# Optimization experiments

Hardware: AMD Instinct MI355X
Metric: run time of the kernel (lower is better)

The kernel has to match this reference:

```python
import jax, jax.numpy as jnp
import numpy as np

N_NODES = 50000
N_EDGES = 400000
IN_CH = 7
EMBED = 128
EDGE_DIM = 6


def setup_inputs() -> dict:
    key = jax.random.key(0)
    ks = jax.random.split(key, 10)
    x = jax.random.normal(ks[0], (N_NODES, IN_CH), dtype=jnp.float32)
    edge_index = jax.random.randint(ks[1], (2, N_EDGES), 0, N_NODES, dtype=jnp.int64)
    edge_attr = jax.random.normal(ks[2], (N_EDGES, EDGE_DIM), dtype=jnp.float32)
    # edge MLP params: Linear(6,128) -> GELU -> Linear(128, 7*128)
    s1 = 1.0 / np.sqrt(EDGE_DIM)
    s2 = 1.0 / np.sqrt(EMBED)
    W1 = jax.random.uniform(ks[3], (EDGE_DIM, EMBED), jnp.float32, -s1, s1)
    b1 = jax.random.uniform(ks[4], (EMBED,), jnp.float32, -s1, s1)
    W2 = jax.random.uniform(ks[5], (EMBED, IN_CH * EMBED), jnp.float32, -s2, s2)
    b2 = jax.random.uniform(ks[6], (IN_CH * EMBED,), jnp.float32, -s2, s2)
    # NNConv root weight and bias
    s3 = 1.0 / np.sqrt(IN_CH)
    root = jax.random.uniform(ks[7], (IN_CH, EMBED), jnp.float32, -s3, s3)
    bias = jnp.zeros((EMBED,), dtype=jnp.float32)
    return {"x": x, "edge_index": edge_index, "edge_attr": edge_attr,
            "W1": W1, "b1": b1, "W2": W2, "b2": b2, "root": root, "bias": bias}


def reference(x, edge_index, edge_attr, W1, b1, W2, b2, root, bias):
    N = x.shape[0]
    src, dst = edge_index[0], edge_index[1]
    # edge MLP -> per-edge weight matrix [E, in_ch, embed]
    h = jax.nn.gelu(edge_attr @ W1 + b1, approximate=False)
    w = (h @ W2 + b2).reshape(-1, IN_CH, EMBED)
    # gather source node features, per-edge small matmul
    msg = jnp.einsum('ei,eio->eo', x[src], w)  # [E, embed]
    # mean aggregation at target nodes
    summed = jax.ops.segment_sum(msg, dst, num_segments=N)
    cnt = jax.ops.segment_sum(jnp.ones((msg.shape[0],), msg.dtype), dst, num_segments=N)
    aggr = summed / jnp.clip(cnt, 1.0)[:, None]
    return aggr + x @ root + bias
```

## Files before the change

kernel.cpp:

```cpp
#include <hip/hip_runtime.h>
#include <stdint.h>

#define NNODES 50000
#define NEDGES 400000
#define INCH 7
#define EMB 128
#define EDIM 6
#define KD 896
#define BM 128
#define NSTEPS 28

typedef __attribute__((ext_vector_type(8))) short bf16x8;
typedef __attribute__((ext_vector_type(4))) float f32x4;

__device__ __forceinline__ short f2bf(float f) {
  union { float f; uint32_t u; } v; v.f = f;
  uint32_t r = v.u + 0x7FFFu + ((v.u >> 16) & 1u);
  return (short)(r >> 16);
}

__global__ void prep_B(const float* __restrict__ W2, short* __restrict__ Bg) {
  int idx = blockIdx.x * 256 + threadIdx.x;
  int o = idx / KD;
  int c = idx - o * KD;
  int i = c >> 7, k = c & 127;
  Bg[idx] = f2bf(W2[k * KD + (i << 7) + o]);
}

__device__ __forceinline__ void stageB(short* dstB, const short* __restrict__ Bg,
                                       int step, int w, int lane) {
#pragma unroll
  for (int j = 0; j < 2; ++j) {
    const int row = w * 32 + j * 16 + (lane >> 2);
    const char* g = (const char*)Bg + (size_t)row * (KD * 2) + step * 64 + (lane & 3) * 16;
    char* l = (char*)dstB + (w * 32 + j * 16) * 64;
    __builtin_amdgcn_global_load_lds((const __attribute__((address_space(1))) void*)g,
                                     (__attribute__((address_space(3))) void*)l,
                                     16, 0, 0);
  }
}

__global__ __launch_bounds__(256, 2)
void nnconv_main(const float* __restrict__ x,
                 const int* __restrict__ ei,
                 const float* __restrict__ ea,
                 const float* __restrict__ W1,
                 const float* __restrict__ b1,
                 const float* __restrict__ b2,
                 const short* __restrict__ Bg,
                 float* __restrict__ cnt,
                 float* __restrict__ out) {
  __shared__ __align__(16) short h_s[BM * EMB];
  __shared__ __align__(16) short B_s[2][EMB * 32];
  __shared__ __align__(16) float x_s[BM][8];
  __shared__ __align__(16) float ea_s[BM * EDIM];
  __shared__ __align__(16) float w1_s[EDIM * EMB];
  __shared__ __align__(16) float b1_s[EMB];
  __shared__ __align__(16) float b2_s[KD];
  __shared__ int dst_s[BM];

  const int t = threadIdx.x;
  const int lane = t & 63;
  const int w = t >> 6;
  const int eb = blockIdx.x * BM;

  if (t < 192) {
    *(float4*)&ea_s[t * 4] = *(const float4*)&ea[(size_t)eb * EDIM + t * 4];
    *(float4*)&w1_s[t * 4] = *(const float4*)&W1[t * 4];
  }
  if (t >= 192 && t < 224) { int q = t - 192; *(float4*)&b1_s[q * 4] = *(const float4*)&b1[q * 4]; }
  if (t < 224) *(float4*)&b2_s[t * 4] = *(const float4*)&b2[t * 4];
  if (t < BM) {
    int s = ei[eb + t];
    int d = ei[NEDGES + eb + t];
    dst_s[t] = d;
#pragma unroll
    for (int i = 0; i < 7; ++i) x_s[t][i] = x[s * 7 + i];
    atomicAdd(&cnt[d], 1.0f);
  }
  stageB(&B_s[0][0], Bg, 0, w, lane);
  __syncthreads();

  {
    const int e = t >> 1, half = t & 1;
    float a[6];
#pragma unroll
    for (int q = 0; q < 6; ++q) a[q] = ea_s[e * 6 + q];
    const int swz = (e & 7) << 4;
#pragma unroll
    for (int j = 0; j < 8; ++j) {
      bf16x8 hv;
#pragma unroll
      for (int m = 0; m < 8; ++m) {
        int c = half * 64 + j * 8 + m;
        float pre = b1_s[c];
#pragma unroll
        for (int q = 0; q < 6; ++q) pre += a[q] * w1_s[q * EMB + c];
        float g = 0.5f * pre * (1.0f + erff(pre * 0.70710678118f));
        hv[m] = f2bf(g);
      }
      int addr = e * 256 + ((half * 128 + j * 16) ^ swz);
      *(bf16x8*)((char*)h_s + addr) = hv;
    }
  }
  asm volatile("s_waitcnt vmcnt(0)" ::: "memory");
  __syncthreads();

  const int wm = w >> 1, wn = w & 1;
  const int rowA = lane & 15;
  const int kseg = lane >> 4;

  f32x4 acc[4][4];
#pragma unroll
  for (int fm = 0; fm < 4; ++fm)
#pragma unroll
    for (int fn = 0; fn < 4; ++fn) acc[fm][fn] = f32x4{0.f, 0.f, 0.f, 0.f};

  int cur = 0;
#pragma unroll 1
  for (int i = 0; i < 7; ++i) {
    f32x4 tmp[4][4];
#pragma unroll
    for (int fm = 0; fm < 4; ++fm)
#pragma unroll
      for (int fn = 0; fn < 4; ++fn) tmp[fm][fn] = f32x4{0.f, 0.f, 0.f, 0.f};

#pragma unroll
    for (int kk = 0; kk < 4; ++kk) {
      const int step = i * 4 + kk;
      if (step < NSTEPS - 1) stageB(&B_s[cur ^ 1][0], Bg, step + 1, w, lane);

      bf16x8 af[4], bfr[4];
#pragma unroll
      for (int fm = 0; fm < 4; ++fm) {
        int row = wm * 64 + fm * 16 + rowA;
        int col = (kk * 64 + kseg * 16) ^ ((row & 7) << 4);
        af[fm] = *(const bf16x8*)((const char*)h_s + row * 256 + col);
      }
#pragma unroll
      for (int fn = 0; fn < 4; ++fn) {
        int n = wn * 64 + fn * 16 + rowA;
        bfr[fn] = *(const bf16x8*)((const char*)&B_s[cur][0] + n * 64 + kseg * 16);
      }
#pragma unroll
      for (int fm = 0; fm < 4; ++fm)
#pragma unroll
        for (int fn = 0; fn < 4; ++fn)
          tmp[fm][fn] = __builtin_amdgcn_mfma_f32_16x16x32_bf16(af[fm], bfr[fn], tmp[fm][fn], 0, 0, 0);

      asm volatile("s_waitcnt vmcnt(0)" ::: "memory");
      __syncthreads();
      cur ^= 1;
    }
#pragma unroll
    for (int fm = 0; fm < 4; ++fm) {
#pragma unroll
      for (int r = 0; r < 4; ++r) {
        float xv = x_s[wm * 64 + fm * 16 + kseg * 4 + r][i];
#pragma unroll
        for (int fn = 0; fn < 4; ++fn) acc[fm][fn][r] += xv * tmp[fm][fn][r];
      }
    }
  }

  const int colA = rowA;
  float bb[4][7];
#pragma unroll
  for (int fn = 0; fn < 4; ++fn)
#pragma unroll
    for (int i = 0; i < 7; ++i) bb[fn][i] = b2_s[i * EMB + wn * 64 + fn * 16 + colA];

#pragma unroll
  for (int fm = 0; fm < 4; ++fm) {
#pragma unroll
    for (int r = 0; r < 4; ++r) {
      const int row = wm * 64 + fm * 16 + kseg * 4 + r;
      float xr[7];
#pragma unroll
      for (int i = 0; i < 7; ++i) xr[i] = x_s[row][i];
      const int d = dst_s[row];
      float* op = out + (size_t)d * EMB + wn * 64 + colA;
#pragma unroll
      for (int fn = 0; fn < 4; ++fn) {
        float v = acc[fm][fn][r];
#pragma unroll
        for (int i = 0; i < 7; ++i) v += xr[i] * bb[fn][i];
        atomicAdd(op + fn * 16, v);
      }
    }
  }
}

__global__ void finalize(const float* __restrict__ x, const float* __restrict__ root,
                         const float* __restrict__ bias, const float* __restrict__ cnt,
                         float* __restrict__ out) {
  int idx = blockIdx.x * 256 + threadIdx.x;
  int n = idx >> 7, o = idx & 127;
  float c = fmaxf(cnt[n], 1.0f);
  float v = out[idx] / c + bias[o];
#pragma unroll
  for (int i = 0; i < 7; ++i) v += x[n * 7 + i] * root[i * EMB + o];
  out[idx] = v;
}

extern "C" void kernel_launch(void* const* d_in, const int* in_sizes, int n_in,
                              void* d_out, int out_size, void* d_ws, size_t ws_size,
                              hipStream_t stream) {
  const float* x    = (const float*)d_in[0];
  const int*   ei   = (const int*)d_in[1];
  const float* ea   = (const float*)d_in[2];
  const float* W1   = (const float*)d_in[3];
  const float* b1   = (const float*)d_in[4];
  const float* W2   = (const float*)d_in[5];
  const float* b2   = (const float*)d_in[6];
  const float* root = (const float*)d_in[7];
  const float* bias = (const float*)d_in[8];
  float* out = (float*)d_out;

  short* Bg  = (short*)d_ws;
  float* cnt = (float*)((char*)d_ws + 128 * KD * 2);

  hipMemsetAsync(out, 0, (size_t)NNODES * EMB * sizeof(float), stream);
  hipMemsetAsync(cnt, 0, (size_t)NNODES * sizeof(float), stream);
  prep_B<<<448, 256, 0, stream>>>(W2, Bg);
  nnconv_main<<<NEDGES / BM, 256, 0, stream>>>(x, ei, ea, W1, b1, b2, Bg, cnt, out);
  finalize<<<NNODES * EMB / 256, 256, 0, stream>>>(x, root, bias, cnt, out);
}
```

Measured before the change: 363.3 us.

## Load pre-swizzled B fragments directly to registers and use tanh GELU

The prep kernel now writes W2 in MFMA fragment order, so each lane can load its B operand straight from global/L2 into registers with double-buffered prefetch. This removes the LDS staging of B and the per-k-step barriers. GELU switches from erf to a tanh approximation built on __expf, which cuts transcendental cost but changes numerics slightly. The h_s swizzle is widened to 16 rows and x_s is padded to reduce LDS bank conflicts.

```diff
diff --git a/kernel.cpp b/kernel.cpp
--- a/kernel.cpp
+++ b/kernel.cpp
@@ -19,25 +19,25 @@
   return (short)(r >> 16);
 }
 
-__global__ void prep_B(const float* __restrict__ W2, short* __restrict__ Bg) {
+__device__ __forceinline__ float fast_gelu(float x) {
+  float x2 = x * x;
+  float y = x * (0.7978845608f + 0.03567740814f * x2);
+  float e = __expf(2.0f * y);
+  float t = 1.0f - 2.0f / (1.0f + e);
+  return 0.5f * x * (1.0f + t);
+}
+
+__global__ void prep_B(const float* __restrict__ W2, short* __restrict__ Bp) {
   int idx = blockIdx.x * 256 + threadIdx.x;
-  int o = idx / KD;
-  int c = idx - o * KD;
-  int i = c >> 7, k = c & 127;
-  Bg[idx] = f2bf(W2[k * KD + (i << 7) + o]);
-}
-
-__device__ __forceinline__ void stageB(short* dstB, const short* __restrict__ Bg,
-                                       int step, int w, int lane) {
-#pragma unroll
-  for (int j = 0; j < 2; ++j) {
-    const int row = w * 32 + j * 16 + (lane >> 2);
-    const char* g = (const char*)Bg + (size_t)row * (KD * 2) + step * 64 + (lane & 3) * 16;
-    char* l = (char*)dstB + (w * 32 + j * 16) * 64;
-    __builtin_amdgcn_global_load_lds((const __attribute__((address_space(1))) void*)g,
-                                     (__attribute__((address_space(3))) void*)l,
-                                     16, 0, 0);
-  }
+  int m    = idx & 7;
+  int r    = (idx >> 3) & 15;
+  int kseg = (idx >> 7) & 3;
+  int nh   = (idx >> 9) & 7;
+  int step = idx >> 12;
+  int i = step >> 2, kk = step & 3;
+  int k = kk * 32 + kseg * 8 + m;
+  int o = nh * 16 + r;
+  Bp[idx] = f2bf(W2[k * KD + i * EMB + o]);
 }
 
 __global__ __launch_bounds__(256, 2)
@@ -47,12 +47,11 @@
                  const float* __restrict__ W1,
                  const float* __restrict__ b1,
                  const float* __restrict__ b2,
-                 const short* __restrict__ Bg,
+                 const short* __restrict__ Bp,
                  float* __restrict__ cnt,
                  float* __restrict__ out) {
   __shared__ __align__(16) short h_s[BM * EMB];
-  __shared__ __align__(16) short B_s[2][EMB * 32];
-  __shared__ __align__(16) float x_s[BM][8];
+  __shared__ __align__(16) float x_s[BM][9];
   __shared__ __align__(16) float ea_s[BM * EDIM];
   __shared__ __align__(16) float w1_s[EDIM * EMB];
   __shared__ __align__(16) float b1_s[EMB];
@@ -78,7 +77,6 @@
     for (int i = 0; i < 7; ++i) x_s[t][i] = x[s * 7 + i];
     atomicAdd(&cnt[d], 1.0f);
   }
-  stageB(&B_s[0][0], Bg, 0, w, lane);
   __syncthreads();
 
   {
@@ -86,7 +84,7 @@
     float a[6];
 #pragma unroll
     for (int q = 0; q < 6; ++q) a[q] = ea_s[e * 6 + q];
-    const int swz = (e & 7) << 4;
+    const int swz = (e & 15) << 4;
 #pragma unroll
     for (int j = 0; j < 8; ++j) {
       bf16x8 hv;
@@ -96,19 +94,18 @@
         float pre = b1_s[c];
 #pragma unroll
         for (int q = 0; q < 6; ++q) pre += a[q] * w1_s[q * EMB + c];
-        float g = 0.5f * pre * (1.0f + erff(pre * 0.70710678118f));
-        hv[m] = f2bf(g);
+        hv[m] = f2bf(fast_gelu(pre));
       }
       int addr = e * 256 + ((half * 128 + j * 16) ^ swz);
       *(bf16x8*)((char*)h_s + addr) = hv;
     }
   }
-  asm volatile("s_waitcnt vmcnt(0)" ::: "memory");
   __syncthreads();
 
   const int wm = w >> 1, wn = w & 1;
   const int rowA = lane & 15;
   const int kseg = lane >> 4;
+  const char* BpByte = (const char*)Bp + (size_t)lane * 16;
 
   f32x4 acc[4][4];
 #pragma unroll
@@ -116,7 +113,11 @@
 #pragma unroll
     for (int fn = 0; fn < 4; ++fn) acc[fm][fn] = f32x4{0.f, 0.f, 0.f, 0.f};
 
-  int cur = 0;
+  bf16x8 bcur[4], bnxt[4];
+#pragma unroll
+  for (int fn = 0; fn < 4; ++fn)
+    bcur[fn] = *(const bf16x8*)(BpByte + ((0 * 8 + wn * 4 + fn) << 10));
+
 #pragma unroll 1
   for (int i = 0; i < 7; ++i) {
     f32x4 tmp[4][4];
@@ -128,29 +129,25 @@
 #pragma unroll
     for (int kk = 0; kk < 4; ++kk) {
       const int step = i * 4 + kk;
-      if (step < NSTEPS - 1) stageB(&B_s[cur ^ 1][0], Bg, step + 1, w, lane);
-
-      bf16x8 af[4], bfr[4];
+      if (step < NSTEPS - 1) {
+#pragma unroll
+        for (int fn = 0; fn < 4; ++fn)
+          bnxt[fn] = *(const bf16x8*)(BpByte + (((step + 1) * 8 + wn * 4 + fn) << 10));
+      }
+      bf16x8 af[4];
 #pragma unroll
       for (int fm = 0; fm < 4; ++fm) {
         int row = wm * 64 + fm * 16 + rowA;
-        int col = (kk * 64 + kseg * 16) ^ ((row & 7) << 4);
+        int col = (kk * 64 + kseg * 16) ^ ((row & 15) << 4);
         af[fm] = *(const bf16x8*)((const char*)h_s + row * 256 + col);
       }
 #pragma unroll
-      for (int fn = 0; fn < 4; ++fn) {
-        int n = wn * 64 + fn * 16 + rowA;
-        bfr[fn] = *(const bf16x8*)((const char*)&B_s[cur][0] + n * 64 + kseg * 16);
-      }
-#pragma unroll
       for (int fm = 0; fm < 4; ++fm)
 #pragma unroll
         for (int fn = 0; fn < 4; ++fn)
-          tmp[fm][fn] = __builtin_amdgcn_mfma_f32_16x16x32_bf16(af[fm], bfr[fn], tmp[fm][fn], 0, 0, 0);
-
-      asm volatile("s_waitcnt vmcnt(0)" ::: "memory");
-      __syncthreads();
-      cur ^= 1;
+          tmp[fm][fn] = __builtin_amdgcn_mfma_f32_16x16x32_bf16(af[fm], bcur[fn], tmp[fm][fn], 0, 0, 0);
+#pragma unroll
+      for (int fn = 0; fn < 4; ++fn) bcur[fn] = bnxt[fn];
     }
 #pragma unroll
     for (int fm = 0; fm < 4; ++fm) {
@@ -217,12 +214,12 @@
   const float* bias = (const float*)d_in[8];
   float* out = (float*)d_out;
 
-  short* Bg  = (short*)d_ws;
+  short* Bp  = (short*)d_ws;
   float* cnt = (float*)((char*)d_ws + 128 * KD * 2);
 
   hipMemsetAsync(out, 0, (size_t)NNODES * EMB * sizeof(float), stream);
   hipMemsetAsync(cnt, 0, (size_t)NNODES * sizeof(float), stream);
-  prep_B<<<448, 256, 0, stream>>>(W2, Bg);
-  nnconv_main<<<NEDGES / BM, 256, 0, stream>>>(x, ei, ea, W1, b1, b2, Bg, cnt, out);
+  prep_B<<<448, 256, 0, stream>>>(W2, Bp);
+  nnconv_main<<<NEDGES / BM, 256, 0, stream>>>(x, ei, ea, W1, b1, b2, Bp, cnt, out);
   finalize<<<NNODES * EMB / 256, 256, 0, stream>>>(x, root, bias, cnt, out);
 }
```

New measurement: 313.1 us. -13.8%, faster.
